# Kernel optimization log

Measured on AMD Instinct MI355X. Metric: run time of the kernel, lower is better.

The kernel has to match this reference:

```python
import jax, jax.numpy as jnp
import numpy as np

NUM_TABLES = 16
NUM_EMBEDDINGS = 200000
EMBED_DIM = 64
BATCH = 4096
POOL = 20  # indices per bag


def setup_inputs() -> dict:
    key = jax.random.key(0)
    k_w, k_i = jax.random.split(key)
    weights = jax.random.normal(
        k_w, (NUM_EMBEDDINGS, NUM_TABLES, EMBED_DIM), dtype=jnp.float32)
    n_idx = NUM_TABLES * BATCH * POOL
    sharded_sparse_features = jax.random.randint(
        k_i, (n_idx,), 0, NUM_EMBEDDINGS, dtype=jnp.int64)
    # offsets delimit T*B bags of length POOL each (fixed pooling factor)
    sharded_offsets = (jnp.arange(NUM_TABLES * BATCH + 1, dtype=jnp.int64) * POOL)
    return {
        "weights": weights,
        "sharded_sparse_features": sharded_sparse_features,
        "sharded_offsets": sharded_offsets,
    }


def reference(weights, sharded_sparse_features, sharded_offsets):
    # weights: [E, T, D]; indices: [N]; offsets: [T*B + 1]
    # bag b of table t covers indices[offsets[t*B + b] : offsets[t*B + b + 1]]
    # output[b, t, :] = sum of weights[idx, t, :] over that bag (sum pooling)
    n_idx = sharded_sparse_features.shape[0]
    num_bags = sharded_offsets.shape[0] - 1  # T * B
    T = weights.shape[1]
    B = num_bags // T
    # segment id (= bag id) of each index position
    seg = jnp.searchsorted(sharded_offsets, jnp.arange(n_idx), side="right") - 1
    table_ids = seg // B  # which table each index belongs to
    rows = weights[sharded_sparse_features, table_ids]  # [N, D] gather
    pooled = jax.ops.segment_sum(rows, seg, num_segments=num_bags)  # [T*B, D]
    return pooled.reshape(T, B, -1).transpose(1, 0, 2)  # [B, T, D]
```

## Files before the change

kernel.cpp:

```cpp
#include <hip/hip_runtime.h>


constexpr int T_TABLES = 16;
constexpr int EMB_D    = 64;

__global__ __launch_bounds__(256)
void embag_kernel(const float* __restrict__ W,
                  const int*   __restrict__ indices,
                  const int*   __restrict__ offsets,
                  float*       __restrict__ out,
                  int B, int num_bags)
{
    const int wave = threadIdx.x >> 6;
    const int lane = threadIdx.x & 63;
    const int g = blockIdx.x * 4 + wave;
    if (g >= num_bags) return;

    const int t = g / B;
    const int b = g - t * B;

    const int start = offsets[g];
    const int end   = offsets[g + 1];

    const float* __restrict__ wbase = W + (size_t)t * EMB_D + lane;
    const size_t row_stride = (size_t)T_TABLES * EMB_D;

    float acc = 0.0f;
    int j = start;
    for (; j + 4 <= end; j += 4) {
        const int i0 = indices[j + 0];
        const int i1 = indices[j + 1];
        const int i2 = indices[j + 2];
        const int i3 = indices[j + 3];
        const float v0 = wbase[(size_t)i0 * row_stride];
        const float v1 = wbase[(size_t)i1 * row_stride];
        const float v2 = wbase[(size_t)i2 * row_stride];
        const float v3 = wbase[(size_t)i3 * row_stride];
        acc += (v0 + v1) + (v2 + v3);
    }
    for (; j < end; ++j) {
        acc += wbase[(size_t)indices[j] * row_stride];
    }

    out[((size_t)b * T_TABLES + t) * EMB_D + lane] = acc;
}

extern "C" void kernel_launch(void* const* d_in, const int* in_sizes, int n_in,
                              void* d_out, int out_size, void* d_ws, size_t ws_size,
                              hipStream_t stream) {
    const float* W       = (const float*)d_in[0];
    const int*   indices = (const int*)d_in[1];
    const int*   offsets = (const int*)d_in[2];
    float*       out     = (float*)d_out;

    const int num_bags = in_sizes[2] - 1;
    const int B = num_bags / T_TABLES;

    const int bags_per_block = 4;
    const int grid = (num_bags + bags_per_block - 1) / bags_per_block;

    embag_kernel<<<grid, 256, 0, stream>>>(W, indices, offsets, out, B, num_bags);
}
```

Measured before the change: 66.46 us.

## Gather embedding rows as float4 across four row groups per wave

Each wave now splits its 64 lanes into 4 groups of 16. Each lane loads a float4, so every group fetches whole 256-byte rows for a different subset of the bag's indices. The partial sums are then combined with cross-lane shuffles. A fully unrolled fast path handles bags of length 20, which puts all five gathers per lane in flight at once. This is meant to cut load instructions and raise memory-level parallelism, at the cost of extra shuffles and only a quarter of the lanes doing the store.

```diff
diff --git a/kernel.cpp b/kernel.cpp
--- a/kernel.cpp
+++ b/kernel.cpp
@@ -3,12 +3,14 @@
 
 constexpr int T_TABLES = 16;
 constexpr int EMB_D    = 64;
+constexpr int D4       = EMB_D / 4;
+constexpr int ROW_F4   = T_TABLES * D4;
 
 __global__ __launch_bounds__(256)
-void embag_kernel(const float* __restrict__ W,
-                  const int*   __restrict__ indices,
-                  const int*   __restrict__ offsets,
-                  float*       __restrict__ out,
+void embag_kernel(const float4* __restrict__ W4,
+                  const int*    __restrict__ indices,
+                  const int*    __restrict__ offsets,
+                  float4*       __restrict__ out4,
                   int B, int num_bags)
 {
     const int wave = threadIdx.x >> 6;
@@ -21,37 +23,58 @@
 
     const int start = offsets[g];
     const int end   = offsets[g + 1];
+    const int n     = end - start;
 
-    const float* __restrict__ wbase = W + (size_t)t * EMB_D + lane;
-    const size_t row_stride = (size_t)T_TABLES * EMB_D;
+    const int r = lane >> 4;
+    const int c = lane & 15;
 
-    float acc = 0.0f;
-    int j = start;
-    for (; j + 4 <= end; j += 4) {
-        const int i0 = indices[j + 0];
-        const int i1 = indices[j + 1];
-        const int i2 = indices[j + 2];
-        const int i3 = indices[j + 3];
-        const float v0 = wbase[(size_t)i0 * row_stride];
-        const float v1 = wbase[(size_t)i1 * row_stride];
-        const float v2 = wbase[(size_t)i2 * row_stride];
-        const float v3 = wbase[(size_t)i3 * row_stride];
-        acc += (v0 + v1) + (v2 + v3);
-    }
-    for (; j < end; ++j) {
-        acc += wbase[(size_t)indices[j] * row_stride];
+    const float4* __restrict__ wbase = W4 + (size_t)t * D4 + c;
+
+    float ax = 0.f, ay = 0.f, az = 0.f, aw = 0.f;
+
+    if (n == 20) {
+        const int j0 = start + r;
+        const int i0 = indices[j0];
+        const int i1 = indices[j0 + 4];
+        const int i2 = indices[j0 + 8];
+        const int i3 = indices[j0 + 12];
+        const int i4 = indices[j0 + 16];
+        const float4 v0 = wbase[(size_t)i0 * ROW_F4];
+        const float4 v1 = wbase[(size_t)i1 * ROW_F4];
+        const float4 v2 = wbase[(size_t)i2 * ROW_F4];
+        const float4 v3 = wbase[(size_t)i3 * ROW_F4];
+        const float4 v4 = wbase[(size_t)i4 * ROW_F4];
+        ax = ((v0.x + v1.x) + (v2.x + v3.x)) + v4.x;
+        ay = ((v0.y + v1.y) + (v2.y + v3.y)) + v4.y;
+        az = ((v0.z + v1.z) + (v2.z + v3.z)) + v4.z;
+        aw = ((v0.w + v1.w) + (v2.w + v3.w)) + v4.w;
+    } else {
+        for (int j = start + r; j < end; j += 4) {
+            const int i = indices[j];
+            const float4 v = wbase[(size_t)i * ROW_F4];
+            ax += v.x; ay += v.y; az += v.z; aw += v.w;
+        }
     }
 
-    out[((size_t)b * T_TABLES + t) * EMB_D + lane] = acc;
+    ax += __shfl_xor(ax, 16); ay += __shfl_xor(ay, 16);
+    az += __shfl_xor(az, 16); aw += __shfl_xor(aw, 16);
+    ax += __shfl_xor(ax, 32); ay += __shfl_xor(ay, 32);
+    az += __shfl_xor(az, 32); aw += __shfl_xor(aw, 32);
+
+    if (r == 0) {
+        float4 acc;
+        acc.x = ax; acc.y = ay; acc.z = az; acc.w = aw;
+        out4[((size_t)b * T_TABLES + t) * D4 + c] = acc;
+    }
 }
 
 extern "C" void kernel_launch(void* const* d_in, const int* in_sizes, int n_in,
                               void* d_out, int out_size, void* d_ws, size_t ws_size,
                               hipStream_t stream) {
-    const float* W       = (const float*)d_in[0];
-    const int*   indices = (const int*)d_in[1];
-    const int*   offsets = (const int*)d_in[2];
-    float*       out     = (float*)d_out;
+    const float4* W4      = (const float4*)d_in[0];
+    const int*    indices = (const int*)d_in[1];
+    const int*    offsets = (const int*)d_in[2];
+    float4*       out4    = (float4*)d_out;
 
     const int num_bags = in_sizes[2] - 1;
     const int B = num_bags / T_TABLES;
@@ -59,5 +82,5 @@
     const int bags_per_block = 4;
     const int grid = (num_bags + bags_per_block - 1) / bags_per_block;
 
-    embag_kernel<<<grid, 256, 0, stream>>>(W, indices, offsets, out, B, num_bags);
+    embag_kernel<<<grid, 256, 0, stream>>>(W4, indices, offsets, out4, B, num_bags);
 }
```

Measured after the change: 56.05 us. 15.7% less time.
